# Optimization experiments

Measured on AMD Instinct MI355X. Metric: run time of the kernel, lower is better.

## Reference

```python
import jax, jax.numpy as jnp
import numpy as np

B, T, IN, H, L, CS, OUT = 256, 256, 256, 1024, 8, 10, 64
CHUNK = H // L


def setup_inputs() -> dict:
    key = jax.random.key(0)
    ks = jax.random.split(key, 16)
    G = 4 * H + 2 * L
    s = 0.05
    return {
        "x": jax.random.normal(ks[0], (B, T, IN), jnp.float32),
        "time": jax.random.uniform(ks[1], (B, T, 1), jnp.float32),
        "kernel_w": jax.random.normal(ks[2], (IN + 1, G), jnp.float32) * s,
        "kernel_b": jnp.zeros((G,), jnp.float32),
        "rec_w": jax.random.normal(ks[3], (H + 1, G), jnp.float32) * s,
        "rec_b": jnp.zeros((G,), jnp.float32),
        "scale_w": jax.random.normal(ks[4], (H, H // 6), jnp.float32) * s,
        "scale_b": jnp.zeros((H // 6,), jnp.float32),
        "rescale_w": jax.random.normal(ks[5], (H // 6, H), jnp.float32) * s,
        "rescale_b": jnp.zeros((H,), jnp.float32),
        "conv_w": jax.random.normal(ks[6], (H, H, CS), jnp.float32) * s,  # (out_ch, in_ch, k)
        "conv_b": jnp.zeros((H,), jnp.float32),
        "out_w": jax.random.normal(ks[7], (H, OUT), jnp.float32) * s,
        "out_b": jnp.zeros((OUT,), jnp.float32),
    }


def _stagenet(x, time, kernel_w, kernel_b, rec_w, rec_b, scale_w, scale_b,
              rescale_w, rescale_b, conv_w, conv_b, out_w, out_b):
    batch = x.shape[0]

    def step(carry, xt):
        c, h, tmp_h, tmp_dis = carry
        inp, intv = xt  # (B,IN), (B,1)
        xo = (jnp.concatenate([inp, intv], -1) @ kernel_w + kernel_b
              + jnp.concatenate([h, intv], -1) @ rec_w + rec_b)  # (B, 4H+2L)
        # master gates via cumax
        fm = jnp.cumsum(jax.nn.softmax(xo[:, :L], axis=-1), axis=-1)            # l2r (B,L)
        im_sm = jax.nn.softmax(xo[:, L:2 * L], axis=-1)
        im = jnp.flip(jnp.cumsum(jnp.flip(im_sm, -1), axis=-1), -1)             # r2l (B,L)
        g = xo[:, 2 * L:].reshape(batch, 4 * L, CHUNK)
        f_g = jax.nn.sigmoid(g[:, :L])
        i_g = jax.nn.sigmoid(g[:, L:2 * L])
        o_g = jax.nn.sigmoid(g[:, 2 * L:3 * L])
        c_in = jnp.tanh(g[:, 3 * L:])
        c_l = c.reshape(batch, L, CHUNK)
        fmE, imE = fm[:, :, None], im[:, :, None]
        ov = fmE * imE
        c_new = ov * (f_g * c_l + i_g * c_in) + (fmE - ov) * c_l + (imE - ov) * c_in
        h_new = (o_g * jnp.tanh(c_new)).reshape(batch, H)
        c_new = c_new.reshape(batch, H)
        cur_dis = 1.0 - jnp.mean(fm, -1)                                        # (B,)
        # sliding window buffers
        tmp_h = jnp.concatenate([tmp_h[1:], h_new[None]], 0)                    # (CS,B,H)
        tmp_dis = jnp.concatenate([tmp_dis[1:], cur_dis[None]], 0)              # (CS,B)
        # cumsum-softmax local attention over the window
        ld = jax.nn.softmax(jnp.cumsum(tmp_dis.T, axis=1), axis=1)              # (B,CS)
        lh = tmp_h.transpose(1, 2, 0) * ld[:, None, :]                          # (B,H,CS)
        theme = jnp.mean(lh, -1) @ scale_w + scale_b
        theme = jax.nn.sigmoid(jax.nn.relu(theme) @ rescale_w + rescale_b)      # (B,H)
        conv_out = jnp.einsum('bck,ock->bo', lh, conv_w) + conv_b               # conv1d, out len 1
        local_h = theme * conv_out
        return (c_new, h_new, tmp_h, tmp_dis), (h_new, local_h, cur_dis)

    c0 = jnp.zeros((batch, H), x.dtype)
    h0 = jnp.zeros((batch, H), x.dtype)
    tmp_h0 = jnp.zeros((CS, batch, H), x.dtype)
    tmp_dis0 = jnp.zeros((CS, batch), x.dtype)
    xs = (x.transpose(1, 0, 2), time.transpose(1, 0, 2))
    _, (origin_h, local_h, distance) = jax.lax.scan(step, (c0, h0, tmp_h0, tmp_dis0), xs)
    rnn = (local_h + origin_h).transpose(1, 0, 2)                               # (B,T,H)
    output = jax.nn.sigmoid(rnn @ out_w + out_b)                                # (B,T,OUT)
    return output, distance  # distance: (T,B)


def reference(x, time, kernel_w, kernel_b, rec_w, rec_b, scale_w, scale_b,
              rescale_w, rescale_b, conv_w, conv_b, out_w, out_b):
    return _stagenet(x, time, kernel_w, kernel_b, rec_w, rec_b, scale_w, scale_b,
                     rescale_w, rescale_b, conv_w, conv_b, out_w, out_b)
```

## Files before the change

### kernel.cpp

```cpp
#include <hip/hip_runtime.h>
#include <hip/hip_bf16.h>
#include <math.h>

#define BB 256
#define TT 256
#define INW 256
#define HH 1024
#define LL 8
#define CSW 10
#define OUTW 64
#define GG 4112
#define KH 1024
#define KXP 896
#define NPAD 4224
#define BH (BB * HH)
#define NPANEL 66

typedef __attribute__((ext_vector_type(8))) short short8;
typedef __attribute__((ext_vector_type(4))) float f32x4;

__device__ __forceinline__ float bf2f(ushort u) {
    union { float f; unsigned int i; } v; v.i = ((unsigned int)u) << 16; return v.f;
}
__device__ __forceinline__ ushort f2bf(float f) {
    __hip_bfloat16 h = __float2bfloat16(f);
    return *(ushort*)&h;
}
__device__ __forceinline__ float sigf(float v) { return 1.0f / (1.0f + expf(-v)); }

template<int WR, int WC, int AMODE, int EPI>
__global__ __launch_bounds__(WR * WC * 64) void mm_kernel(
    const ushort* __restrict__ A, const ushort* __restrict__ hR,
    const ushort* __restrict__ hLo,
    const ushort* __restrict__ BT, const float* __restrict__ bias,
    void* __restrict__ Cp, const float* __restrict__ ldw,
    const ushort* __restrict__ TH, float* __restrict__ outp,
    int splitStride, int ldaA, int ldb, int ldc, int K, int t, int RING, int tBase)
{
    constexpr int BM = WR * 64, BN = WC * 64, NT = WR * WC * 64, LS = 72;
    constexpr int AIT = BM * 8 / NT, BIT = BN * 8 / NT;
    __shared__ ushort As[BM * LS];
    __shared__ ushort Bs[BN * LS];
    const int tid = threadIdx.x;
    const int lane = tid & 63, wave = tid >> 6;
    const int wr = wave / WC, wc = wave % WC;

    int bx, by, zSel = 0;
    const ushort* BTeff = BT;
    const ushort* Abase = A;
    if (AMODE == 1) {
        int vid = blockIdx.x;
        int xcd = vid & 7, q = vid >> 3;
        int p = -1, mem = 0;
        for (int j = 0; ; ++j) {
            int pp = xcd + 8 * j;
            if (pp >= NPANEL) break;
            int cc = (pp < 33) ? 4 : 2;
            if (q < cc) { p = pp; mem = q; break; }
            q -= cc;
        }
        if (p < 0) return;
        if (p < 33) { bx = p;      zSel = (mem < 2) ? 0 : 2; by = mem & 1; BTeff = BT; }
        else        { bx = p - 33; zSel = 1;                 by = mem & 1; BTeff = A;  }
        Abase = (zSel == 2) ? hLo : hR + (size_t)((t + 8) % RING) * BH;
    } else if (AMODE == 2) {
        int vid = blockIdx.x;
        bx = (vid >> 3) & 7;
        by = ((vid >> 6) << 3) + (vid & 7);
        if (by >= t) return;
    } else {
        bx = blockIdx.x; by = blockIdx.y;
    }
    const int m0 = by * BM, n0 = bx * BN;
    f32x4 acc[4][4] = {};

    auto gather = [&](int ktl, short8* vA, short8* vB) {
#pragma unroll
        for (int i = 0; i < AIT; ++i) {
            int id = tid + i * NT;
            int r = id >> 3, cc = id & 7;
            int k = ktl + cc * 8;
            short8 v;
            if (AMODE == 0) {
                v = *(const short8*)(A + (size_t)(m0 + r) * ldaA + k);
            } else if (AMODE == 1) {
                v = *(const short8*)(Abase + (size_t)(m0 + r) * HH + k);
            } else {
                int ks = k >> 10, c = k & 1023;
                int tt = m0 >> 8, b = (m0 & 255) + r;
                int slot = (tBase + tt + ks) % RING;
                short8 hv = *(const short8*)(hR + (size_t)slot * BH + (size_t)b * HH + c);
                float s = ldw[((size_t)tt * 256 + b) * CSW + ks];
                ushort* pv = (ushort*)&hv;
                ushort* po = (ushort*)&v;
#pragma unroll
                for (int j = 0; j < 8; ++j) po[j] = f2bf(bf2f(pv[j]) * s);
            }
            vA[i] = v;
        }
#pragma unroll
        for (int i = 0; i < BIT; ++i) {
            int id = tid + i * NT;
            int n = id >> 3, cc = id & 7;
            vB[i] = *(const short8*)(BTeff + (size_t)(n0 + n) * ldb + ktl + cc * 8);
        }
    };

    short8 vA[AIT], vB[BIT];
    gather(0, vA, vB);

    for (int kt = 0; kt < K; kt += 64) {
#pragma unroll
        for (int i = 0; i < AIT; ++i) {
            int id = tid + i * NT;
            *(short8*)(As + (id >> 3) * LS + (id & 7) * 8) = vA[i];
        }
#pragma unroll
        for (int i = 0; i < BIT; ++i) {
            int id = tid + i * NT;
            *(short8*)(Bs + (id >> 3) * LS + (id & 7) * 8) = vB[i];
        }
        __syncthreads();
        if (kt + 64 < K) gather(kt + 64, vA, vB);
#pragma unroll
        for (int kf = 0; kf < 2; ++kf) {
            short8 aF[4], bF[4];
#pragma unroll
            for (int mi = 0; mi < 4; ++mi)
                aF[mi] = *(const short8*)(As + (wr * 64 + mi * 16 + (lane & 15)) * LS + kf * 32 + (lane >> 4) * 8);
#pragma unroll
            for (int ni = 0; ni < 4; ++ni)
                bF[ni] = *(const short8*)(Bs + (wc * 64 + ni * 16 + (lane & 15)) * LS + kf * 32 + (lane >> 4) * 8);
#pragma unroll
            for (int mi = 0; mi < 4; ++mi)
#pragma unroll
                for (int ni = 0; ni < 4; ++ni)
                    acc[mi][ni] = __builtin_amdgcn_mfma_f32_16x16x32_bf16(aF[mi], bF[ni], acc[mi][ni], 0, 0, 0);
        }
        __syncthreads();
    }
#pragma unroll
    for (int mi = 0; mi < 4; ++mi) {
#pragma unroll
        for (int ni = 0; ni < 4; ++ni) {
#pragma unroll
            for (int j = 0; j < 4; ++j) {
                int row = m0 + wr * 64 + mi * 16 + ((lane >> 4) << 2) + j;
                int col = n0 + wc * 64 + ni * 16 + (lane & 15);
                float v = acc[mi][ni][j];
                if (EPI != 0 && bias) v += bias[col];
                if (EPI == 0) {
                    ((float*)Cp)[(size_t)zSel * splitStride + (size_t)row * ldc + col] = v;
                } else if (EPI == 1) {
                    ((ushort*)Cp)[(size_t)row * ldc + col] = f2bf(v > 0.f ? v : 0.f);
                } else if (EPI == 2) {
                    ((ushort*)Cp)[(size_t)row * ldc + col] = f2bf(sigf(v));
                } else if (EPI == 3) {
                    int tt = row >> 8, b = row & 255;
                    int slot = (tBase + tt + 9) % RING;
                    float th = bf2f(TH[(size_t)row * HH + col]);
                    float h  = bf2f(hR[(size_t)slot * BH + (size_t)b * HH + col]);
                    ((ushort*)Cp)[(size_t)row * ldc + col] = f2bf(th * v + h);
                } else {
                    int tt = tBase + (row >> 8), b = row & 255;
                    outp[((size_t)b * TT + tt) * OUTW + col] = sigf(v);
                }
            }
        }
    }
}

__global__ void build_whl(const float* __restrict__ rw,
                          ushort* __restrict__ WhiT, ushort* __restrict__ WloT)
{
    size_t i = (size_t)blockIdx.x * 256 + threadIdx.x;
    if (i >= (size_t)NPAD * KH) return;
    int n = (int)(i / KH), k = (int)(i % KH);
    float w = (n < GG) ? rw[(size_t)k * GG + n] : 0.f;
    ushort hi = f2bf(w);
    WhiT[i] = hi;
    WloT[i] = f2bf(w - bf2f(hi));
}

__global__ void build_wxt(const float* __restrict__ kw, const float* __restrict__ rw,
                          ushort* __restrict__ WxT)
{
    size_t i = (size_t)blockIdx.x * 256 + threadIdx.x;
    if (i >= (size_t)NPAD * KXP) return;
    int n = (int)(i / KXP), k = (int)(i % KXP);
    int seg = k / 288, kk = k - seg * 288;
    float w = 0.f;
    if (n < GG && seg < 3) {
        if (kk < 256)      w = kw[(size_t)kk * GG + n];
        else if (kk == 256) w = kw[(size_t)256 * GG + n];
        else if (kk == 257) w = rw[(size_t)1024 * GG + n];
    }
    ushort hi = f2bf(w);
    WxT[i] = (seg == 1) ? f2bf(w - bf2f(hi)) : hi;
}

__global__ void build_bc(const float* __restrict__ kb, const float* __restrict__ rb,
                         float* __restrict__ bc)
{
    int i = blockIdx.x * 256 + threadIdx.x;
    if (i < NPAD) bc[i] = (i < GG) ? kb[i] + rb[i] : 0.f;
}

__global__ void build_xac(const float* __restrict__ x, const float* __restrict__ tim,
                          ushort* __restrict__ XAc, int tBase, int Mloc)
{
    size_t i = (size_t)blockIdx.x * 256 + threadIdx.x;
    if (i >= (size_t)Mloc * KXP) return;
    int m = (int)(i / KXP), k = (int)(i % KXP);
    int t = tBase + (m >> 8), b = m & 255;
    int seg = k / 288, kk = k - seg * 288;
    float v = 0.f;
    if (seg < 3) {
        if (kk < 256)       v = x[((size_t)b * TT + t) * INW + kk];
        else if (kk < 258)  v = tim[(size_t)b * TT + t];
    }
    ushort hi = f2bf(v);
    XAc[i] = (seg == 2) ? f2bf(v - bf2f(hi)) : hi;
}

__global__ void build_ctt(const float* __restrict__ cw, ushort* __restrict__ ctT)
{
    size_t i = (size_t)blockIdx.x * 256 + threadIdx.x;
    if (i >= (size_t)HH * HH * CSW) return;
    int o = (int)(i / (HH * CSW)), rest = (int)(i % (HH * CSW));
    int k = rest >> 10, c = rest & 1023;
    ctT[i] = f2bf(cw[((size_t)o * HH + c) * CSW + k]);
}

__global__ void build_swt(const float* __restrict__ sw, const float* __restrict__ sb,
                          ushort* __restrict__ swT, float* __restrict__ sbP)
{
    int i = blockIdx.x * 256 + threadIdx.x;
    if (i < 256 * 1024) {
        int n = i >> 10, k = i & 1023;
        swT[i] = f2bf(n < 170 ? sw[(size_t)k * 170 + n] : 0.f);
    }
    if (i < 256) sbP[i] = (i < 170) ? sb[i] : 0.f;
}

__global__ void build_rswt(const float* __restrict__ rsw, ushort* __restrict__ rswT)
{
    int i = blockIdx.x * 256 + threadIdx.x;
    if (i >= 1024 * 256) return;
    int n = i >> 8, k = i & 255;
    rswT[i] = f2bf(k < 170 ? rsw[(size_t)k * HH + n] : 0.f);
}

__global__ void build_owt(const float* __restrict__ ow, ushort* __restrict__ owT)
{
    int i = blockIdx.x * 256 + threadIdx.x;
    if (i >= OUTW * HH) return;
    int n = i >> 10, k = i & 1023;
    owT[i] = f2bf(ow[(size_t)k * OUTW + n]);
}

__global__ __launch_bounds__(256) void step_kernel(
    const float* __restrict__ xoP, const float* __restrict__ xoX,
    const float* __restrict__ bc,
    float* __restrict__ c, ushort* __restrict__ hR, ushort* __restrict__ hLo,
    float* __restrict__ dist, int t, int tBase, int RING)
{
    const size_t S = (size_t)BB * NPAD;
    int b = blockIdx.x, tid = threadIdx.x;
    const float* x0 = xoP + (size_t)b * NPAD;
    const float* xx = xoX + ((size_t)(t - tBase) * 256 + b) * NPAD;
    __shared__ float fm[LL], im[LL];
    if (tid == 0) {
        float xr[2 * LL];
        for (int l = 0; l < 2 * LL; ++l)
            xr[l] = x0[l] + x0[S + l] + x0[2 * S + l] + xx[l] + bc[l];
        float m1 = -1e30f, m2 = -1e30f;
        for (int l = 0; l < LL; ++l) { m1 = fmaxf(m1, xr[l]); m2 = fmaxf(m2, xr[LL + l]); }
        float e1[LL], e2[LL], s1 = 0.f, s2 = 0.f;
        for (int l = 0; l < LL; ++l) {
            e1[l] = expf(xr[l] - m1); s1 += e1[l];
            e2[l] = expf(xr[LL + l] - m2); s2 += e2[l];
        }
        float cum = 0.f, mean = 0.f;
        for (int l = 0; l < LL; ++l) { cum += e1[l] / s1; fm[l] = cum; mean += cum; }
        float rc = 0.f;
        for (int l = LL - 1; l >= 0; --l) { rc += e2[l] / s2; im[l] = rc; }
        dist[(size_t)t * BB + b] = 1.0f - mean / LL;
    }
    __syncthreads();
    int slot = (t + 9) % RING;
    for (int e = tid; e < HH; e += 256) {
        int l = e >> 7;
        int c0 = 2 * LL + e;
        float f  = sigf(x0[c0] + x0[S + c0] + x0[2 * S + c0] + xx[c0] + bc[c0]);
        int c1 = c0 + HH;
        float ig = sigf(x0[c1] + x0[S + c1] + x0[2 * S + c1] + xx[c1] + bc[c1]);
        int c2 = c1 + HH;
        float og = sigf(x0[c2] + x0[S + c2] + x0[2 * S + c2] + xx[c2] + bc[c2]);
        int c3 = c2 + HH;
        float ci = tanhf(x0[c3] + x0[S + c3] + x0[2 * S + c3] + xx[c3] + bc[c3]);
        size_t idx = (size_t)b * HH + e;
        float cl = c[idx];
        float F = fm[l], I = im[l], OV = F * I;
        float cn = OV * (f * cl + ig * ci) + (F - OV) * cl + (I - OV) * ci;
        float hn = og * tanhf(cn);
        c[idx] = cn;
        ushort hi = f2bf(hn);
        hR[(size_t)slot * BH + idx] = hi;
        hLo[idx] = f2bf(hn - bf2f(hi));
    }
}

__global__ void ld_chunk_kernel(const float* __restrict__ dist, float* __restrict__ ldC,
                                int tBase, int Mloc)
{
    int id = blockIdx.x * 256 + threadIdx.x;
    if (id >= Mloc) return;
    int t = tBase + (id >> 8), b = id & 255;
    float cv[CSW], cum = 0.f, mx = -1e30f;
#pragma unroll
    for (int k = 0; k < CSW; ++k) {
        int ts = t - 9 + k;
        cum += (ts >= 0) ? dist[(size_t)ts * BB + b] : 0.f;
        cv[k] = cum; mx = fmaxf(mx, cum);
    }
    float ss = 0.f;
#pragma unroll
    for (int k = 0; k < CSW; ++k) { cv[k] = expf(cv[k] - mx); ss += cv[k]; }
    float inv = 1.0f / ss;
#pragma unroll
    for (int k = 0; k < CSW; ++k) ldC[(size_t)id * CSW + k] = cv[k] * inv;
}

__global__ void mlh_kernel(const ushort* __restrict__ hR, const float* __restrict__ ldC,
                           ushort* __restrict__ MLH, int tBase, int RING)
{
    size_t id = (size_t)blockIdx.x * 256 + threadIdx.x;
    int m = (int)(id >> 7);
    int c0 = ((int)(id & 127)) << 3;
    int t = tBase + (m >> 8), b = m & 255;
    float acc[8] = {};
#pragma unroll
    for (int k = 0; k < CSW; ++k) {
        float s = ldC[(size_t)m * CSW + k];
        int slot = (t + k) % RING;
        short8 hv = *(const short8*)(hR + (size_t)slot * BH + (size_t)b * HH + c0);
        ushort* pv = (ushort*)&hv;
#pragma unroll
        for (int j = 0; j < 8; ++j) acc[j] += bf2f(pv[j]) * s;
    }
#pragma unroll
    for (int j = 0; j < 8; ++j) MLH[(size_t)m * HH + c0 + j] = f2bf(acc[j] * 0.1f);
}

extern "C" void kernel_launch(void* const* d_in, const int* in_sizes, int n_in,
                              void* d_out, int out_size, void* d_ws, size_t ws_size,
                              hipStream_t stream)
{
    const float* x   = (const float*)d_in[0];
    const float* tim = (const float*)d_in[1];
    const float* kw  = (const float*)d_in[2];
    const float* kb  = (const float*)d_in[3];
    const float* rw  = (const float*)d_in[4];
    const float* rb  = (const float*)d_in[5];
    const float* sw  = (const float*)d_in[6];
    const float* sb  = (const float*)d_in[7];
    const float* rsw = (const float*)d_in[8];
    const float* rsb = (const float*)d_in[9];
    const float* cw  = (const float*)d_in[10];
    const float* cb  = (const float*)d_in[11];
    const float* ow  = (const float*)d_in[12];
    const float* ob  = (const float*)d_in[13];
    float* out  = (float*)d_out;
    float* dist = out + (size_t)BB * TT * OUTW;

    auto planSize = [&](int tch) -> size_t {
        size_t o = 0;
        auto al = [&](size_t bytes) { o += (bytes + 255) & ~(size_t)255; };
        int ring = tch + 9;
        al((size_t)ring * BH * 2);
        al((size_t)BH * 2);
        al((size_t)BH * 4);
        al((size_t)NPAD * KH * 2);
        al((size_t)NPAD * KH * 2);
        al((size_t)NPAD * KXP * 2);
        al((size_t)NPAD * 4);
        al((size_t)3 * BB * NPAD * 4);
        al((size_t)tch * 256 * NPAD * 4);
        al((size_t)tch * 256 * KXP * 2);
        al((size_t)tch * 256 * CSW * 4);
        al((size_t)HH * HH * CSW * 2);
        al((size_t)256 * 1024 * 2);
        al((size_t)256 * 4);
        al((size_t)1024 * 256 * 2);
        al((size_t)OUTW * HH * 2);
        al((size_t)tch * 256 * HH * 2);
        al((size_t)tch * 256 * 256 * 2);
        al((size_t)tch * 256 * HH * 2);
        return o;
    };
    const int cands[5] = {32, 16, 8, 4, 2};
    int TCH = 0;
    for (int ci = 0; ci < 5; ++ci)
        if (planSize(cands[ci]) <= ws_size) { TCH = cands[ci]; break; }
    if (TCH == 0) return;
    const int RING = TCH + 9;
    const int Mloc = TCH * 256;
    const int nM = Mloc / 128;

    char* base = (char*)d_ws;
    size_t off = 0;
    auto alloc = [&](size_t bytes) { char* p = base + off; off += (bytes + 255) & ~(size_t)255; return p; };
    ushort* hRing = (ushort*)alloc((size_t)RING * BH * 2);
    ushort* hLo   = (ushort*)alloc((size_t)BH * 2);
    float*  c     = (float*) alloc((size_t)BH * 4);
    ushort* WhiT  = (ushort*)alloc((size_t)NPAD * KH * 2);
    ushort* WloT  = (ushort*)alloc((size_t)NPAD * KH * 2);
    ushort* WxT   = (ushort*)alloc((size_t)NPAD * KXP * 2);
    float*  bc    = (float*) alloc((size_t)NPAD * 4);
    float*  xoP   = (float*) alloc((size_t)3 * BB * NPAD * 4);
    float*  xoX   = (float*) alloc((size_t)Mloc * NPAD * 4);
    ushort* XAc   = (ushort*)alloc((size_t)Mloc * KXP * 2);
    float*  ldC   = (float*) alloc((size_t)Mloc * CSW * 4);
    ushort* ctT   = (ushort*)alloc((size_t)HH * HH * CSW * 2);
    ushort* swT   = (ushort*)alloc((size_t)256 * 1024 * 2);
    float*  sbP   = (float*) alloc((size_t)256 * 4);
    ushort* rswT  = (ushort*)alloc((size_t)1024 * 256 * 2);
    ushort* owT   = (ushort*)alloc((size_t)OUTW * HH * 2);
    ushort* MLH   = (ushort*)alloc((size_t)Mloc * HH * 2);
    ushort* TH1   = (ushort*)alloc((size_t)Mloc * 256 * 2);
    ushort* TH    = (ushort*)alloc((size_t)Mloc * HH * 2);
    ushort* RNN   = MLH;

    hipMemsetAsync(hRing, 0, (size_t)9 * BH * 2, stream);
    hipMemsetAsync(hLo, 0, (size_t)BH * 2, stream);
    hipMemsetAsync(c, 0, (size_t)BH * 4, stream);

    build_whl<<<(int)(((size_t)NPAD * KH + 255) / 256), 256, 0, stream>>>(rw, WhiT, WloT);
    build_wxt<<<(int)(((size_t)NPAD * KXP + 255) / 256), 256, 0, stream>>>(kw, rw, WxT);
    build_bc<<<(NPAD + 255) / 256, 256, 0, stream>>>(kb, rb, bc);
    build_ctt<<<(int)(((size_t)HH * HH * CSW + 255) / 256), 256, 0, stream>>>(cw, ctT);
    build_swt<<<(256 * 1024 + 255) / 256, 256, 0, stream>>>(sw, sb, swT, sbP);
    build_rswt<<<(1024 * 256 + 255) / 256, 256, 0, stream>>>(rsw, rswT);
    build_owt<<<(OUTW * HH + 255) / 256, 256, 0, stream>>>(ow, owT);

    const int SPLIT_STRIDE = BB * NPAD;

    for (int tBase = 0; tBase < TT; tBase += TCH) {
        build_xac<<<(int)(((size_t)Mloc * KXP + 255) / 256), 256, 0, stream>>>(
            x, tim, XAc, tBase, Mloc);
        mm_kernel<2, 2, 0, 0><<<dim3(33, Mloc / 128), 256, 0, stream>>>(
            XAc, nullptr, nullptr, WxT, nullptr, xoX, nullptr, nullptr, nullptr,
            0, KXP, KXP, NPAD, KXP, 0, RING, tBase);
        for (int t = tBase; t < tBase + TCH; ++t) {
            mm_kernel<2, 2, 1, 0><<<dim3(224), 256, 0, stream>>>(
                WloT, hRing, hLo, WhiT, nullptr, xoP, nullptr, nullptr, nullptr,
                SPLIT_STRIDE, 0, KH, NPAD, KH, t, RING, 0);
            step_kernel<<<BB, 256, 0, stream>>>(
                xoP, xoX, bc, c, hRing, hLo, dist, t, tBase, RING);
        }
        ld_chunk_kernel<<<(Mloc + 255) / 256, 256, 0, stream>>>(dist, ldC, tBase, Mloc);
        mlh_kernel<<<Mloc / 2, 256, 0, stream>>>(hRing, ldC, MLH, tBase, RING);
        mm_kernel<2, 2, 0, 1><<<dim3(2, Mloc / 128), 256, 0, stream>>>(
            MLH, nullptr, nullptr, swT, sbP, TH1, nullptr, nullptr, nullptr,
            0, 1024, 1024, 256, 1024, 0, RING, tBase);
        mm_kernel<2, 2, 0, 2><<<dim3(8, Mloc / 128), 256, 0, stream>>>(
            TH1, nullptr, nullptr, rswT, rsb, TH, nullptr, nullptr, nullptr,
            0, 256, 256, 1024, 256, 0, RING, tBase);
        mm_kernel<2, 2, 2, 3><<<dim3(((nM + 7) / 8) * 64), 256, 0, stream>>>(
            nullptr, hRing, nullptr, ctT, cb, RNN, ldC, TH, nullptr,
            0, 0, HH * CSW, 1024, HH * CSW, nM, RING, tBase);
        mm_kernel<4, 1, 0, 4><<<dim3(1, Mloc / 256), 256, 0, stream>>>(
            RNN, nullptr, nullptr, owT, ob, nullptr, nullptr, nullptr, out,
            0, 1024, 1024, 0, 1024, 0, RING, tBase);
    }
}
```

Baseline: 13.05 ms.

## Fuse per-timestep recurrent GEMM and gate step into persistent grid-barrier scan kernel

Replaces the two launches per timestep (the split recurrent GEMM and the gate update) with one persistent kernel per time chunk. Blocks synchronise through atomic grid barriers, and the gate update runs on 256 blocks between barriers. The work split also changes: each hi-weight block now does a K-half with both hi and lo h operands, and the lo-weight blocks do the full K. This removes per-step launch overhead and kernel-boundary drains. It relies on all 256 blocks being co-resident, or the barrier deadlocks, and spin-waits on global atomics.

```diff
diff --git a/kernel.cpp b/kernel.cpp
--- a/kernel.cpp
+++ b/kernel.cpp
@@ -14,7 +14,6 @@
 #define KXP 896
 #define NPAD 4224
 #define BH (BB * HH)
-#define NPANEL 66
 
 typedef __attribute__((ext_vector_type(8))) short short8;
 typedef __attribute__((ext_vector_type(4))) float f32x4;
@@ -27,6 +26,176 @@
     return *(ushort*)&h;
 }
 __device__ __forceinline__ float sigf(float v) { return 1.0f / (1.0f + expf(-v)); }
+
+__device__ __forceinline__ void grid_barrier(unsigned int* bar, int idx, int nblk)
+{
+    __syncthreads();
+    if (threadIdx.x == 0) {
+        __threadfence();
+        __hip_atomic_fetch_add(&bar[idx], 1u, __ATOMIC_ACQ_REL, __HIP_MEMORY_SCOPE_AGENT);
+        while (__hip_atomic_load(&bar[idx], __ATOMIC_RELAXED, __HIP_MEMORY_SCOPE_AGENT) < (unsigned int)nblk)
+            __builtin_amdgcn_s_sleep(4);
+        __threadfence();
+    }
+    __syncthreads();
+}
+
+__global__ __launch_bounds__(256) void scan_kernel(
+    const ushort* __restrict__ WhiT, const ushort* __restrict__ WloT,
+    ushort* __restrict__ hR, ushort* __restrict__ hLo, float* __restrict__ cSt,
+    const float* __restrict__ xoX, const float* __restrict__ bc,
+    float* __restrict__ xoP, float* __restrict__ dist,
+    unsigned int* __restrict__ bar, int tBase, int TCH, int RING, int NBLK)
+{
+    constexpr int LS = 72;
+    __shared__ ushort Bs[128 * LS];
+    __shared__ ushort Ahs[128 * LS];
+    __shared__ ushort Als[128 * LS];
+    __shared__ float fmS[LL], imS[LL];
+
+    const int tid = threadIdx.x;
+    const int lane = tid & 63, wave = tid >> 6;
+    const int wr = wave >> 1, wc = wave & 1;
+    const int bid = blockIdx.x;
+
+    int xcd = bid & 7, q = bid >> 3;
+    int p = -1, mem = 0;
+    for (int j = 0; ; ++j) {
+        int pp = xcd + 8 * j;
+        if (pp >= 66) break;
+        int cc = (pp < 33) ? 4 : 2;
+        if (q < cc) { p = pp; mem = q; break; }
+        q -= cc;
+    }
+    int nt = 0, mt = 0, kBeg = 0, nIter = 0, pout = 0;
+    bool dual = false;
+    const ushort* Bsrc = WhiT;
+    if (p >= 0) {
+        if (p < 33) { nt = p;      mt = mem >> 1; kBeg = (mem & 1) * 512; nIter = 8;  pout = mem & 1; dual = true;  Bsrc = WhiT; }
+        else        { nt = p - 33; mt = mem;      kBeg = 0;               nIter = 16; pout = 2;       dual = false; Bsrc = WloT; }
+    }
+    const int m0 = mt * 128, n0 = nt * 128;
+    const size_t SPL = (size_t)BB * NPAD;
+
+    for (int tt = 0; tt < TCH; ++tt) {
+        const int t = tBase + tt;
+        if (p >= 0) {
+            const ushort* AhiG = hR + (size_t)((t + 8) % RING) * BH;
+            f32x4 acc[4][4] = {};
+            short8 vB[4], vH[4], vL[4];
+            auto gath = [&](int kt) {
+#pragma unroll
+                for (int i = 0; i < 4; ++i) {
+                    int id = tid + i * 256;
+                    int r = id >> 3, c8 = id & 7;
+                    int k = kBeg + kt + c8 * 8;
+                    vB[i] = *(const short8*)(Bsrc + (size_t)(n0 + r) * KH + k);
+                    vH[i] = *(const short8*)(AhiG + (size_t)(m0 + r) * HH + k);
+                    if (dual) vL[i] = *(const short8*)(hLo + (size_t)(m0 + r) * HH + k);
+                }
+            };
+            gath(0);
+            for (int it = 0; it < nIter; ++it) {
+#pragma unroll
+                for (int i = 0; i < 4; ++i) {
+                    int id = tid + i * 256;
+                    int r = id >> 3, c8 = id & 7;
+                    *(short8*)(Bs + r * LS + c8 * 8) = vB[i];
+                    *(short8*)(Ahs + r * LS + c8 * 8) = vH[i];
+                    if (dual) *(short8*)(Als + r * LS + c8 * 8) = vL[i];
+                }
+                __syncthreads();
+                if (it + 1 < nIter) gath((it + 1) * 64);
+#pragma unroll
+                for (int kf = 0; kf < 2; ++kf) {
+                    short8 aH[4], bF[4];
+#pragma unroll
+                    for (int mi = 0; mi < 4; ++mi)
+                        aH[mi] = *(const short8*)(Ahs + (wr * 64 + mi * 16 + (lane & 15)) * LS + kf * 32 + (lane >> 4) * 8);
+#pragma unroll
+                    for (int ni = 0; ni < 4; ++ni)
+                        bF[ni] = *(const short8*)(Bs + (wc * 64 + ni * 16 + (lane & 15)) * LS + kf * 32 + (lane >> 4) * 8);
+#pragma unroll
+                    for (int mi = 0; mi < 4; ++mi)
+#pragma unroll
+                        for (int ni = 0; ni < 4; ++ni)
+                            acc[mi][ni] = __builtin_amdgcn_mfma_f32_16x16x32_bf16(aH[mi], bF[ni], acc[mi][ni], 0, 0, 0);
+                    if (dual) {
+                        short8 aL[4];
+#pragma unroll
+                        for (int mi = 0; mi < 4; ++mi)
+                            aL[mi] = *(const short8*)(Als + (wr * 64 + mi * 16 + (lane & 15)) * LS + kf * 32 + (lane >> 4) * 8);
+#pragma unroll
+                        for (int mi = 0; mi < 4; ++mi)
+#pragma unroll
+                            for (int ni = 0; ni < 4; ++ni)
+                                acc[mi][ni] = __builtin_amdgcn_mfma_f32_16x16x32_bf16(aL[mi], bF[ni], acc[mi][ni], 0, 0, 0);
+                    }
+                }
+                __syncthreads();
+            }
+            float* dst = xoP + (size_t)pout * SPL;
+#pragma unroll
+            for (int mi = 0; mi < 4; ++mi)
+#pragma unroll
+                for (int ni = 0; ni < 4; ++ni)
+#pragma unroll
+                    for (int j = 0; j < 4; ++j) {
+                        int row = m0 + wr * 64 + mi * 16 + ((lane >> 4) << 2) + j;
+                        int col = n0 + wc * 64 + ni * 16 + (lane & 15);
+                        dst[(size_t)row * NPAD + col] = acc[mi][ni][j];
+                    }
+        }
+        grid_barrier(bar, 2 * tt, NBLK);
+        if (bid < BB) {
+            int b = bid;
+            const float* p0 = xoP + (size_t)b * NPAD;
+            const float* p1 = p0 + SPL;
+            const float* p2 = p1 + SPL;
+            const float* xx = xoX + ((size_t)tt * 256 + b) * NPAD;
+            if (tid == 0) {
+                float xr[2 * LL];
+                for (int l = 0; l < 2 * LL; ++l)
+                    xr[l] = p0[l] + p1[l] + p2[l] + xx[l] + bc[l];
+                float m1 = -1e30f, m2 = -1e30f;
+                for (int l = 0; l < LL; ++l) { m1 = fmaxf(m1, xr[l]); m2 = fmaxf(m2, xr[LL + l]); }
+                float e1[LL], e2[LL], s1 = 0.f, s2 = 0.f;
+                for (int l = 0; l < LL; ++l) {
+                    e1[l] = expf(xr[l] - m1); s1 += e1[l];
+                    e2[l] = expf(xr[LL + l] - m2); s2 += e2[l];
+                }
+                float cum = 0.f, mean = 0.f;
+                for (int l = 0; l < LL; ++l) { cum += e1[l] / s1; fmS[l] = cum; mean += cum; }
+                float rc = 0.f;
+                for (int l = LL - 1; l >= 0; --l) { rc += e2[l] / s2; imS[l] = rc; }
+                dist[(size_t)t * BB + b] = 1.0f - mean / LL;
+            }
+            __syncthreads();
+            int slot = (t + 9) % RING;
+            for (int e = tid; e < HH; e += 256) {
+                int l = e >> 7;
+                int c0 = 2 * LL + e;
+                float f  = sigf(p0[c0] + p1[c0] + p2[c0] + xx[c0] + bc[c0]);
+                int c1 = c0 + HH;
+                float ig = sigf(p0[c1] + p1[c1] + p2[c1] + xx[c1] + bc[c1]);
+                int c2 = c1 + HH;
+                float og = sigf(p0[c2] + p1[c2] + p2[c2] + xx[c2] + bc[c2]);
+                int c3 = c2 + HH;
+                float ci = tanhf(p0[c3] + p1[c3] + p2[c3] + xx[c3] + bc[c3]);
+                size_t idx = (size_t)b * HH + e;
+                float cl = cSt[idx];
+                float F = fmS[l], I = imS[l], OV = F * I;
+                float cn = OV * (f * cl + ig * ci) + (F - OV) * cl + (I - OV) * ci;
+                float hn = og * tanhf(cn);
+                cSt[idx] = cn;
+                ushort hi = f2bf(hn);
+                hR[(size_t)slot * BH + idx] = hi;
+                hLo[idx] = f2bf(hn - bf2f(hi));
+            }
+        }
+        grid_barrier(bar, 2 * tt + 1, NBLK);
+    }
+}
 
 template<int WR, int WC, int AMODE, int EPI>
 __global__ __launch_bounds__(WR * WC * 64) void mm_kernel(
@@ -45,25 +214,8 @@
     const int lane = tid & 63, wave = tid >> 6;
     const int wr = wave / WC, wc = wave % WC;
 
-    int bx, by, zSel = 0;
-    const ushort* BTeff = BT;
-    const ushort* Abase = A;
-    if (AMODE == 1) {
-        int vid = blockIdx.x;
-        int xcd = vid & 7, q = vid >> 3;
-        int p = -1, mem = 0;
-        for (int j = 0; ; ++j) {
-            int pp = xcd + 8 * j;
-            if (pp >= NPANEL) break;
-            int cc = (pp < 33) ? 4 : 2;
-            if (q < cc) { p = pp; mem = q; break; }
-            q -= cc;
-        }
-        if (p < 0) return;
-        if (p < 33) { bx = p;      zSel = (mem < 2) ? 0 : 2; by = mem & 1; BTeff = BT; }
-        else        { bx = p - 33; zSel = 1;                 by = mem & 1; BTeff = A;  }
-        Abase = (zSel == 2) ? hLo : hR + (size_t)((t + 8) % RING) * BH;
-    } else if (AMODE == 2) {
+    int bx, by;
+    if (AMODE == 2) {
         int vid = blockIdx.x;
         bx = (vid >> 3) & 7;
         by = ((vid >> 6) << 3) + (vid & 7);
@@ -83,8 +235,6 @@
             short8 v;
             if (AMODE == 0) {
                 v = *(const short8*)(A + (size_t)(m0 + r) * ldaA + k);
-            } else if (AMODE == 1) {
-                v = *(const short8*)(Abase + (size_t)(m0 + r) * HH + k);
             } else {
                 int ks = k >> 10, c = k & 1023;
                 int tt = m0 >> 8, b = (m0 & 255) + r;
@@ -102,7 +252,7 @@
         for (int i = 0; i < BIT; ++i) {
             int id = tid + i * NT;
             int n = id >> 3, cc = id & 7;
-            vB[i] = *(const short8*)(BTeff + (size_t)(n0 + n) * ldb + ktl + cc * 8);
+            vB[i] = *(const short8*)(BT + (size_t)(n0 + n) * ldb + ktl + cc * 8);
         }
     };
 
@@ -150,7 +300,7 @@
                 float v = acc[mi][ni][j];
                 if (EPI != 0 && bias) v += bias[col];
                 if (EPI == 0) {
-                    ((float*)Cp)[(size_t)zSel * splitStride + (size_t)row * ldc + col] = v;
+                    ((float*)Cp)[(size_t)row * ldc + col] = v;
                 } else if (EPI == 1) {
                     ((ushort*)Cp)[(size_t)row * ldc + col] = f2bf(v > 0.f ? v : 0.f);
                 } else if (EPI == 2) {
@@ -191,7 +341,7 @@
     int seg = k / 288, kk = k - seg * 288;
     float w = 0.f;
     if (n < GG && seg < 3) {
-        if (kk < 256)      w = kw[(size_t)kk * GG + n];
+        if (kk < 256)       w = kw[(size_t)kk * GG + n];
         else if (kk == 256) w = kw[(size_t)256 * GG + n];
         else if (kk == 257) w = rw[(size_t)1024 * GG + n];
     }
@@ -257,58 +407,6 @@
     if (i >= OUTW * HH) return;
     int n = i >> 10, k = i & 1023;
     owT[i] = f2bf(ow[(size_t)k * OUTW + n]);
-}
-
-__global__ __launch_bounds__(256) void step_kernel(
-    const float* __restrict__ xoP, const float* __restrict__ xoX,
-    const float* __restrict__ bc,
-    float* __restrict__ c, ushort* __restrict__ hR, ushort* __restrict__ hLo,
-    float* __restrict__ dist, int t, int tBase, int RING)
-{
-    const size_t S = (size_t)BB * NPAD;
-    int b = blockIdx.x, tid = threadIdx.x;
-    const float* x0 = xoP + (size_t)b * NPAD;
-    const float* xx = xoX + ((size_t)(t - tBase) * 256 + b) * NPAD;
-    __shared__ float fm[LL], im[LL];
-    if (tid == 0) {
-        float xr[2 * LL];
-        for (int l = 0; l < 2 * LL; ++l)
-            xr[l] = x0[l] + x0[S + l] + x0[2 * S + l] + xx[l] + bc[l];
-        float m1 = -1e30f, m2 = -1e30f;
-        for (int l = 0; l < LL; ++l) { m1 = fmaxf(m1, xr[l]); m2 = fmaxf(m2, xr[LL + l]); }
-        float e1[LL], e2[LL], s1 = 0.f, s2 = 0.f;
-        for (int l = 0; l < LL; ++l) {
-            e1[l] = expf(xr[l] - m1); s1 += e1[l];
-            e2[l] = expf(xr[LL + l] - m2); s2 += e2[l];
-        }
-        float cum = 0.f, mean = 0.f;
-        for (int l = 0; l < LL; ++l) { cum += e1[l] / s1; fm[l] = cum; mean += cum; }
-        float rc = 0.f;
-        for (int l = LL - 1; l >= 0; --l) { rc += e2[l] / s2; im[l] = rc; }
-        dist[(size_t)t * BB + b] = 1.0f - mean / LL;
-    }
-    __syncthreads();
-    int slot = (t + 9) % RING;
-    for (int e = tid; e < HH; e += 256) {
-        int l = e >> 7;
-        int c0 = 2 * LL + e;
-        float f  = sigf(x0[c0] + x0[S + c0] + x0[2 * S + c0] + xx[c0] + bc[c0]);
-        int c1 = c0 + HH;
-        float ig = sigf(x0[c1] + x0[S + c1] + x0[2 * S + c1] + xx[c1] + bc[c1]);
-        int c2 = c1 + HH;
-        float og = sigf(x0[c2] + x0[S + c2] + x0[2 * S + c2] + xx[c2] + bc[c2]);
-        int c3 = c2 + HH;
-        float ci = tanhf(x0[c3] + x0[S + c3] + x0[2 * S + c3] + xx[c3] + bc[c3]);
-        size_t idx = (size_t)b * HH + e;
-        float cl = c[idx];
-        float F = fm[l], I = im[l], OV = F * I;
-        float cn = OV * (f * cl + ig * ci) + (F - OV) * cl + (I - OV) * ci;
-        float hn = og * tanhf(cn);
-        c[idx] = cn;
-        ushort hi = f2bf(hn);
-        hR[(size_t)slot * BH + idx] = hi;
-        hLo[idx] = f2bf(hn - bf2f(hi));
-    }
 }
 
 __global__ void ld_chunk_kernel(const float* __restrict__ dist, float* __restrict__ ldC,
@@ -397,6 +495,7 @@
         al((size_t)tch * 256 * HH * 2);
         al((size_t)tch * 256 * 256 * 2);
         al((size_t)tch * 256 * HH * 2);
+        al(1024);
         return o;
     };
     const int cands[5] = {32, 16, 8, 4, 2};
@@ -407,13 +506,14 @@
     const int RING = TCH + 9;
     const int Mloc = TCH * 256;
     const int nM = Mloc / 128;
+    const int NBLK = 256;
 
     char* base = (char*)d_ws;
     size_t off = 0;
     auto alloc = [&](size_t bytes) { char* p = base + off; off += (bytes + 255) & ~(size_t)255; return p; };
     ushort* hRing = (ushort*)alloc((size_t)RING * BH * 2);
     ushort* hLo   = (ushort*)alloc((size_t)BH * 2);
-    float*  c     = (float*) alloc((size_t)BH * 4);
+    float*  cSt   = (float*) alloc((size_t)BH * 4);
     ushort* WhiT  = (ushort*)alloc((size_t)NPAD * KH * 2);
     ushort* WloT  = (ushort*)alloc((size_t)NPAD * KH * 2);
     ushort* WxT   = (ushort*)alloc((size_t)NPAD * KXP * 2);
@@ -430,11 +530,12 @@
     ushort* MLH   = (ushort*)alloc((size_t)Mloc * HH * 2);
     ushort* TH1   = (ushort*)alloc((size_t)Mloc * 256 * 2);
     ushort* TH    = (ushort*)alloc((size_t)Mloc * HH * 2);
+    unsigned int* bar = (unsigned int*)alloc(1024);
     ushort* RNN   = MLH;
 
     hipMemsetAsync(hRing, 0, (size_t)9 * BH * 2, stream);
     hipMemsetAsync(hLo, 0, (size_t)BH * 2, stream);
-    hipMemsetAsync(c, 0, (size_t)BH * 4, stream);
+    hipMemsetAsync(cSt, 0, (size_t)BH * 4, stream);
 
     build_whl<<<(int)(((size_t)NPAD * KH + 255) / 256), 256, 0, stream>>>(rw, WhiT, WloT);
     build_wxt<<<(int)(((size_t)NPAD * KXP + 255) / 256), 256, 0, stream>>>(kw, rw, WxT);
@@ -444,21 +545,16 @@
     build_rswt<<<(1024 * 256 + 255) / 256, 256, 0, stream>>>(rsw, rswT);
     build_owt<<<(OUTW * HH + 255) / 256, 256, 0, stream>>>(ow, owT);
 
-    const int SPLIT_STRIDE = BB * NPAD;
-
     for (int tBase = 0; tBase < TT; tBase += TCH) {
         build_xac<<<(int)(((size_t)Mloc * KXP + 255) / 256), 256, 0, stream>>>(
             x, tim, XAc, tBase, Mloc);
         mm_kernel<2, 2, 0, 0><<<dim3(33, Mloc / 128), 256, 0, stream>>>(
             XAc, nullptr, nullptr, WxT, nullptr, xoX, nullptr, nullptr, nullptr,
             0, KXP, KXP, NPAD, KXP, 0, RING, tBase);
-        for (int t = tBase; t < tBase + TCH; ++t) {
-            mm_kernel<2, 2, 1, 0><<<dim3(224), 256, 0, stream>>>(
-                WloT, hRing, hLo, WhiT, nullptr, xoP, nullptr, nullptr, nullptr,
-                SPLIT_STRIDE, 0, KH, NPAD, KH, t, RING, 0);
-            step_kernel<<<BB, 256, 0, stream>>>(
-                xoP, xoX, bc, c, hRing, hLo, dist, t, tBase, RING);
-        }
+        hipMemsetAsync(bar, 0, (size_t)2 * TCH * 4, stream);
+        scan_kernel<<<NBLK, 256, 0, stream>>>(
+            WhiT, WloT, hRing, hLo, cSt, xoX, bc, xoP, dist, bar,
+            tBase, TCH, RING, NBLK);
         ld_chunk_kernel<<<(Mloc + 255) / 256, 256, 0, stream>>>(dist, ldC, tBase, Mloc);
         mlh_kernel<<<Mloc / 2, 256, 0, stream>>>(hRing, ldC, MLH, tBase, RING);
         mm_kernel<2, 2, 0, 1><<<dim3(2, Mloc / 128), 256, 0, stream>>>(
```

After: 28.12 ms. 2.15x slower.

## Drop low-bf16 weight term and split recurrent GEMM over K halves

Applied to the files above, without the earlier changes.

The recurrent matmul previously computed three split-precision products (h_hi·W_hi, h_lo·W_hi, h_hi·W_lo), each written to its own partial buffer. It now drops the W_lo term and fuses h_hi and h_lo into one tile that shares the W_hi B-fragments. The K dimension is split into two halves, and each half goes to a separate block, so there are two partial outputs instead of three. The input projection and bias are folded into the epilogue of the first K-half, which leaves the step kernel summing only two partials. This cuts weight traffic, partial-buffer traffic and step-kernel reads per timestep. The cost is lower accuracy, since the low-order weight correction is gone, and fewer blocks (160 instead of 224).

```diff
diff --git a/kernel.cpp b/kernel.cpp
--- a/kernel.cpp
+++ b/kernel.cpp
@@ -14,7 +14,7 @@
 #define KXP 896
 #define NPAD 4224
 #define BH (BB * HH)
-#define NPANEL 66
+#define SPL ((size_t)BB * NPAD)
 
 typedef __attribute__((ext_vector_type(8))) short short8;
 typedef __attribute__((ext_vector_type(4))) float f32x4;
@@ -31,38 +31,30 @@
 template<int WR, int WC, int AMODE, int EPI>
 __global__ __launch_bounds__(WR * WC * 64) void mm_kernel(
     const ushort* __restrict__ A, const ushort* __restrict__ hR,
-    const ushort* __restrict__ hLo,
-    const ushort* __restrict__ BT, const float* __restrict__ bias,
-    void* __restrict__ Cp, const float* __restrict__ ldw,
-    const ushort* __restrict__ TH, float* __restrict__ outp,
-    int splitStride, int ldaA, int ldb, int ldc, int K, int t, int RING, int tBase)
+    const ushort* __restrict__ hLo, const ushort* __restrict__ BT,
+    const float* __restrict__ bias, void* __restrict__ Cp,
+    const float* __restrict__ ldw, const ushort* __restrict__ TH,
+    float* __restrict__ outp, const float* __restrict__ xof,
+    int ldaA, int ldb, int ldc, int K, int t, int RING, int tBase, int tLoc)
 {
     constexpr int BM = WR * 64, BN = WC * 64, NT = WR * WC * 64, LS = 72;
     constexpr int AIT = BM * 8 / NT, BIT = BN * 8 / NT;
     __shared__ ushort As[BM * LS];
     __shared__ ushort Bs[BN * LS];
+    __shared__ ushort Als[AMODE == 1 ? BM * LS : 1];
     const int tid = threadIdx.x;
     const int lane = tid & 63, wave = tid >> 6;
     const int wr = wave / WC, wc = wave % WC;
 
-    int bx, by, zSel = 0;
-    const ushort* BTeff = BT;
-    const ushort* Abase = A;
+    int bx, by, kh = 0, kBase = 0;
     if (AMODE == 1) {
         int vid = blockIdx.x;
         int xcd = vid & 7, q = vid >> 3;
-        int p = -1, mem = 0;
-        for (int j = 0; ; ++j) {
-            int pp = xcd + 8 * j;
-            if (pp >= NPANEL) break;
-            int cc = (pp < 33) ? 4 : 2;
-            if (q < cc) { p = pp; mem = q; break; }
-            q -= cc;
-        }
-        if (p < 0) return;
-        if (p < 33) { bx = p;      zSel = (mem < 2) ? 0 : 2; by = mem & 1; BTeff = BT; }
-        else        { bx = p - 33; zSel = 1;                 by = mem & 1; BTeff = A;  }
-        Abase = (zSel == 2) ? hLo : hR + (size_t)((t + 8) % RING) * BH;
+        int p = xcd + 8 * (q >> 2);
+        if (p >= 33) return;
+        int mem = q & 3;
+        by = mem >> 1; kh = mem & 1;
+        bx = p; kBase = kh * 512;
     } else if (AMODE == 2) {
         int vid = blockIdx.x;
         bx = (vid >> 3) & 7;
@@ -74,7 +66,9 @@
     const int m0 = by * BM, n0 = bx * BN;
     f32x4 acc[4][4] = {};
 
-    auto gather = [&](int ktl, short8* vA, short8* vB) {
+    const ushort* Ahi = (AMODE == 1) ? hR + (size_t)((t + 8) % RING) * BH : nullptr;
+
+    auto gather = [&](int ktl, short8* vA, short8* vL, short8* vB) {
 #pragma unroll
         for (int i = 0; i < AIT; ++i) {
             int id = tid + i * NT;
@@ -84,7 +78,8 @@
             if (AMODE == 0) {
                 v = *(const short8*)(A + (size_t)(m0 + r) * ldaA + k);
             } else if (AMODE == 1) {
-                v = *(const short8*)(Abase + (size_t)(m0 + r) * HH + k);
+                v = *(const short8*)(Ahi + (size_t)(m0 + r) * HH + kBase + k);
+                vL[i] = *(const short8*)(hLo + (size_t)(m0 + r) * HH + kBase + k);
             } else {
                 int ks = k >> 10, c = k & 1023;
                 int tt = m0 >> 8, b = (m0 & 255) + r;
@@ -102,18 +97,20 @@
         for (int i = 0; i < BIT; ++i) {
             int id = tid + i * NT;
             int n = id >> 3, cc = id & 7;
-            vB[i] = *(const short8*)(BTeff + (size_t)(n0 + n) * ldb + ktl + cc * 8);
+            vB[i] = *(const short8*)(BT + (size_t)(n0 + n) * ldb + kBase + ktl + cc * 8);
         }
     };
 
-    short8 vA[AIT], vB[BIT];
-    gather(0, vA, vB);
+    short8 vA[AIT], vL[AMODE == 1 ? AIT : 1], vB[BIT];
+    gather(0, vA, vL, vB);
 
     for (int kt = 0; kt < K; kt += 64) {
 #pragma unroll
         for (int i = 0; i < AIT; ++i) {
             int id = tid + i * NT;
             *(short8*)(As + (id >> 3) * LS + (id & 7) * 8) = vA[i];
+            if (AMODE == 1)
+                *(short8*)(Als + (id >> 3) * LS + (id & 7) * 8) = vL[i];
         }
 #pragma unroll
         for (int i = 0; i < BIT; ++i) {
@@ -121,7 +118,7 @@
             *(short8*)(Bs + (id >> 3) * LS + (id & 7) * 8) = vB[i];
         }
         __syncthreads();
-        if (kt + 64 < K) gather(kt + 64, vA, vB);
+        if (kt + 64 < K) gather(kt + 64, vA, vL, vB);
 #pragma unroll
         for (int kf = 0; kf < 2; ++kf) {
             short8 aF[4], bF[4];
@@ -136,6 +133,17 @@
 #pragma unroll
                 for (int ni = 0; ni < 4; ++ni)
                     acc[mi][ni] = __builtin_amdgcn_mfma_f32_16x16x32_bf16(aF[mi], bF[ni], acc[mi][ni], 0, 0, 0);
+            if (AMODE == 1) {
+                short8 aL[4];
+#pragma unroll
+                for (int mi = 0; mi < 4; ++mi)
+                    aL[mi] = *(const short8*)(Als + (wr * 64 + mi * 16 + (lane & 15)) * LS + kf * 32 + (lane >> 4) * 8);
+#pragma unroll
+                for (int mi = 0; mi < 4; ++mi)
+#pragma unroll
+                    for (int ni = 0; ni < 4; ++ni)
+                        acc[mi][ni] = __builtin_amdgcn_mfma_f32_16x16x32_bf16(aL[mi], bF[ni], acc[mi][ni], 0, 0, 0);
+            }
         }
         __syncthreads();
     }
@@ -148,38 +156,40 @@
                 int row = m0 + wr * 64 + mi * 16 + ((lane >> 4) << 2) + j;
                 int col = n0 + wc * 64 + ni * 16 + (lane & 15);
                 float v = acc[mi][ni][j];
-                if (EPI != 0 && bias) v += bias[col];
-                if (EPI == 0) {
-                    ((float*)Cp)[(size_t)zSel * splitStride + (size_t)row * ldc + col] = v;
-                } else if (EPI == 1) {
-                    ((ushort*)Cp)[(size_t)row * ldc + col] = f2bf(v > 0.f ? v : 0.f);
-                } else if (EPI == 2) {
-                    ((ushort*)Cp)[(size_t)row * ldc + col] = f2bf(sigf(v));
-                } else if (EPI == 3) {
-                    int tt = row >> 8, b = row & 255;
-                    int slot = (tBase + tt + 9) % RING;
-                    float th = bf2f(TH[(size_t)row * HH + col]);
-                    float h  = bf2f(hR[(size_t)slot * BH + (size_t)b * HH + col]);
-                    ((ushort*)Cp)[(size_t)row * ldc + col] = f2bf(th * v + h);
+                if (AMODE == 1 && EPI == 0) {
+                    if (kh == 0)
+                        v += xof[((size_t)tLoc * 256 + row) * NPAD + col] + bias[col];
+                    ((float*)Cp)[(size_t)kh * SPL + (size_t)row * ldc + col] = v;
                 } else {
-                    int tt = tBase + (row >> 8), b = row & 255;
-                    outp[((size_t)b * TT + tt) * OUTW + col] = sigf(v);
+                    if (EPI != 0 && bias) v += bias[col];
+                    if (EPI == 0) {
+                        ((float*)Cp)[(size_t)row * ldc + col] = v;
+                    } else if (EPI == 1) {
+                        ((ushort*)Cp)[(size_t)row * ldc + col] = f2bf(v > 0.f ? v : 0.f);
+                    } else if (EPI == 2) {
+                        ((ushort*)Cp)[(size_t)row * ldc + col] = f2bf(sigf(v));
+                    } else if (EPI == 3) {
+                        int tt = row >> 8, b = row & 255;
+                        int slot = (tBase + tt + 9) % RING;
+                        float th = bf2f(TH[(size_t)row * HH + col]);
+                        float h = bf2f(hR[(size_t)slot * BH + (size_t)b * HH + col]);
+                        ((ushort*)Cp)[(size_t)row * ldc + col] = f2bf(th * v + h);
+                    } else {
+                        int tt = tBase + (row >> 8), b = row & 255;
+                        outp[((size_t)b * TT + tt) * OUTW + col] = sigf(v);
+                    }
                 }
             }
         }
     }
 }
 
-__global__ void build_whl(const float* __restrict__ rw,
-                          ushort* __restrict__ WhiT, ushort* __restrict__ WloT)
+__global__ void build_whi(const float* __restrict__ rw, ushort* __restrict__ WhiT)
 {
     size_t i = (size_t)blockIdx.x * 256 + threadIdx.x;
     if (i >= (size_t)NPAD * KH) return;
     int n = (int)(i / KH), k = (int)(i % KH);
-    float w = (n < GG) ? rw[(size_t)k * GG + n] : 0.f;
-    ushort hi = f2bf(w);
-    WhiT[i] = hi;
-    WloT[i] = f2bf(w - bf2f(hi));
+    WhiT[i] = f2bf((n < GG) ? rw[(size_t)k * GG + n] : 0.f);
 }
 
 __global__ void build_wxt(const float* __restrict__ kw, const float* __restrict__ rw,
@@ -191,7 +201,7 @@
     int seg = k / 288, kk = k - seg * 288;
     float w = 0.f;
     if (n < GG && seg < 3) {
-        if (kk < 256)      w = kw[(size_t)kk * GG + n];
+        if (kk < 256)       w = kw[(size_t)kk * GG + n];
         else if (kk == 256) w = kw[(size_t)256 * GG + n];
         else if (kk == 257) w = rw[(size_t)1024 * GG + n];
     }
@@ -216,8 +226,8 @@
     int seg = k / 288, kk = k - seg * 288;
     float v = 0.f;
     if (seg < 3) {
-        if (kk < 256)       v = x[((size_t)b * TT + t) * INW + kk];
-        else if (kk < 258)  v = tim[(size_t)b * TT + t];
+        if (kk < 256)      v = x[((size_t)b * TT + t) * INW + kk];
+        else if (kk < 258) v = tim[(size_t)b * TT + t];
     }
     ushort hi = f2bf(v);
     XAc[i] = (seg == 2) ? f2bf(v - bf2f(hi)) : hi;
@@ -260,20 +270,17 @@
 }
 
 __global__ __launch_bounds__(256) void step_kernel(
-    const float* __restrict__ xoP, const float* __restrict__ xoX,
-    const float* __restrict__ bc,
-    float* __restrict__ c, ushort* __restrict__ hR, ushort* __restrict__ hLo,
-    float* __restrict__ dist, int t, int tBase, int RING)
-{
-    const size_t S = (size_t)BB * NPAD;
+    const float* __restrict__ xoP, float* __restrict__ c,
+    ushort* __restrict__ hR, ushort* __restrict__ hLo,
+    float* __restrict__ dist, int t, int RING)
+{
     int b = blockIdx.x, tid = threadIdx.x;
     const float* x0 = xoP + (size_t)b * NPAD;
-    const float* xx = xoX + ((size_t)(t - tBase) * 256 + b) * NPAD;
+    const float* x1 = x0 + SPL;
     __shared__ float fm[LL], im[LL];
     if (tid == 0) {
         float xr[2 * LL];
-        for (int l = 0; l < 2 * LL; ++l)
-            xr[l] = x0[l] + x0[S + l] + x0[2 * S + l] + xx[l] + bc[l];
+        for (int l = 0; l < 2 * LL; ++l) xr[l] = x0[l] + x1[l];
         float m1 = -1e30f, m2 = -1e30f;
         for (int l = 0; l < LL; ++l) { m1 = fmaxf(m1, xr[l]); m2 = fmaxf(m2, xr[LL + l]); }
         float e1[LL], e2[LL], s1 = 0.f, s2 = 0.f;
@@ -292,13 +299,13 @@
     for (int e = tid; e < HH; e += 256) {
         int l = e >> 7;
         int c0 = 2 * LL + e;
-        float f  = sigf(x0[c0] + x0[S + c0] + x0[2 * S + c0] + xx[c0] + bc[c0]);
+        float f  = sigf(x0[c0] + x1[c0]);
         int c1 = c0 + HH;
-        float ig = sigf(x0[c1] + x0[S + c1] + x0[2 * S + c1] + xx[c1] + bc[c1]);
+        float ig = sigf(x0[c1] + x1[c1]);
         int c2 = c1 + HH;
-        float og = sigf(x0[c2] + x0[S + c2] + x0[2 * S + c2] + xx[c2] + bc[c2]);
+        float og = sigf(x0[c2] + x1[c2]);
         int c3 = c2 + HH;
-        float ci = tanhf(x0[c3] + x0[S + c3] + x0[2 * S + c3] + xx[c3] + bc[c3]);
+        float ci = tanhf(x0[c3] + x1[c3]);
         size_t idx = (size_t)b * HH + e;
         float cl = c[idx];
         float F = fm[l], I = im[l], OV = F * I;
@@ -382,10 +389,9 @@
         al((size_t)BH * 2);
         al((size_t)BH * 4);
         al((size_t)NPAD * KH * 2);
-        al((size_t)NPAD * KH * 2);
         al((size_t)NPAD * KXP * 2);
         al((size_t)NPAD * 4);
-        al((size_t)3 * BB * NPAD * 4);
+        al((size_t)2 * BB * NPAD * 4);
         al((size_t)tch * 256 * NPAD * 4);
         al((size_t)tch * 256 * KXP * 2);
         al((size_t)tch * 256 * CSW * 4);
@@ -415,10 +421,9 @@
     ushort* hLo   = (ushort*)alloc((size_t)BH * 2);
     float*  c     = (float*) alloc((size_t)BH * 4);
     ushort* WhiT  = (ushort*)alloc((size_t)NPAD * KH * 2);
-    ushort* WloT  = (ushort*)alloc((size_t)NPAD * KH * 2);
     ushort* WxT   = (ushort*)alloc((size_t)NPAD * KXP * 2);
     float*  bc    = (float*) alloc((size_t)NPAD * 4);
-    float*  xoP   = (float*) alloc((size_t)3 * BB * NPAD * 4);
+    float*  xoP   = (float*) alloc((size_t)2 * BB * NPAD * 4);
     float*  xoX   = (float*) alloc((size_t)Mloc * NPAD * 4);
     ushort* XAc   = (ushort*)alloc((size_t)Mloc * KXP * 2);
     float*  ldC   = (float*) alloc((size_t)Mloc * CSW * 4);
@@ -436,7 +441,7 @@
     hipMemsetAsync(hLo, 0, (size_t)BH * 2, stream);
     hipMemsetAsync(c, 0, (size_t)BH * 4, stream);
 
-    build_whl<<<(int)(((size_t)NPAD * KH + 255) / 256), 256, 0, stream>>>(rw, WhiT, WloT);
+    build_whi<<<(int)(((size_t)NPAD * KH + 255) / 256), 256, 0, stream>>>(rw, WhiT);
     build_wxt<<<(int)(((size_t)NPAD * KXP + 255) / 256), 256, 0, stream>>>(kw, rw, WxT);
     build_bc<<<(NPAD + 255) / 256, 256, 0, stream>>>(kb, rb, bc);
     build_ctt<<<(int)(((size_t)HH * HH * CSW + 255) / 256), 256, 0, stream>>>(cw, ctT);
@@ -444,34 +449,31 @@
     build_rswt<<<(1024 * 256 + 255) / 256, 256, 0, stream>>>(rsw, rswT);
     build_owt<<<(OUTW * HH + 255) / 256, 256, 0, stream>>>(ow, owT);
 
-    const int SPLIT_STRIDE = BB * NPAD;
-
     for (int tBase = 0; tBase < TT; tBase += TCH) {
         build_xac<<<(int)(((size_t)Mloc * KXP + 255) / 256), 256, 0, stream>>>(
             x, tim, XAc, tBase, Mloc);
         mm_kernel<2, 2, 0, 0><<<dim3(33, Mloc / 128), 256, 0, stream>>>(
-            XAc, nullptr, nullptr, WxT, nullptr, xoX, nullptr, nullptr, nullptr,
-            0, KXP, KXP, NPAD, KXP, 0, RING, tBase);
+            XAc, nullptr, nullptr, WxT, nullptr, xoX, nullptr, nullptr, nullptr, nullptr,
+            KXP, KXP, NPAD, KXP, 0, RING, tBase, 0);
         for (int t = tBase; t < tBase + TCH; ++t) {
-            mm_kernel<2, 2, 1, 0><<<dim3(224), 256, 0, stream>>>(
-                WloT, hRing, hLo, WhiT, nullptr, xoP, nullptr, nullptr, nullptr,
-                SPLIT_STRIDE, 0, KH, NPAD, KH, t, RING, 0);
-            step_kernel<<<BB, 256, 0, stream>>>(
-                xoP, xoX, bc, c, hRing, hLo, dist, t, tBase, RING);
+            mm_kernel<2, 2, 1, 0><<<dim3(160), 256, 0, stream>>>(
+                nullptr, hRing, hLo, WhiT, bc, xoP, nullptr, nullptr, nullptr, xoX,
+                0, KH, NPAD, 512, t, RING, 0, t - tBase);
+            step_kernel<<<BB, 256, 0, stream>>>(xoP, c, hRing, hLo, dist, t, RING);
         }
         ld_chunk_kernel<<<(Mloc + 255) / 256, 256, 0, stream>>>(dist, ldC, tBase, Mloc);
         mlh_kernel<<<Mloc / 2, 256, 0, stream>>>(hRing, ldC, MLH, tBase, RING);
         mm_kernel<2, 2, 0, 1><<<dim3(2, Mloc / 128), 256, 0, stream>>>(
-            MLH, nullptr, nullptr, swT, sbP, TH1, nullptr, nullptr, nullptr,
-            0, 1024, 1024, 256, 1024, 0, RING, tBase);
+            MLH, nullptr, nullptr, swT, sbP, TH1, nullptr, nullptr, nullptr, nullptr,
+            1024, 1024, 256, 1024, 0, RING, tBase, 0);
         mm_kernel<2, 2, 0, 2><<<dim3(8, Mloc / 128), 256, 0, stream>>>(
-            TH1, nullptr, nullptr, rswT, rsb, TH, nullptr, nullptr, nullptr,
-            0, 256, 256, 1024, 256, 0, RING, tBase);
+            TH1, nullptr, nullptr, rswT, rsb, TH, nullptr, nullptr, nullptr, nullptr,
+            256, 256, 1024, 256, 0, RING, tBase, 0);
         mm_kernel<2, 2, 2, 3><<<dim3(((nM + 7) / 8) * 64), 256, 0, stream>>>(
-            nullptr, hRing, nullptr, ctT, cb, RNN, ldC, TH, nullptr,
-            0, 0, HH * CSW, 1024, HH * CSW, nM, RING, tBase);
+            nullptr, hRing, nullptr, ctT, cb, RNN, ldC, TH, nullptr, nullptr,
+            0, HH * CSW, 1024, HH * CSW, nM, RING, tBase, 0);
         mm_kernel<4, 1, 0, 4><<<dim3(1, Mloc / 256), 256, 0, stream>>>(
-            RNN, nullptr, nullptr, owT, ob, nullptr, nullptr, nullptr, out,
-            0, 1024, 1024, 0, 1024, 0, RING, tBase);
-    }
-}
+            RNN, nullptr, nullptr, owT, ob, nullptr, nullptr, nullptr, out, nullptr,
+            1024, 1024, 0, 1024, 0, RING, tBase, 0);
+    }
+}
```

Result: slower. 13.80 ms (+5.7%).
